# Kernel tuning notes

Hardware: AMD Instinct MI355X
Metric: run time of the kernel (lower is better)

Reference implementation:

```python
import jax, jax.numpy as jnp
import numpy as np

U, D, B, E, H = 128, 256, 1024, 64, 8
EPS_LN = 1e-5
FS0 = 1.0 / 137.036


def _ln(h, g, b):
    m = h.mean(-1, keepdims=True)
    v = jnp.var(h, axis=-1, keepdims=True)
    return (h - m) * jax.lax.rsqrt(v + EPS_LN) * g + b


def setup_inputs() -> dict:
    key = jax.random.key(0)
    ks = iter(jax.random.split(key, 40))

    def n(shape, s=0.05):
        return jax.random.normal(next(ks), shape, jnp.float32) * s

    return dict(
        x=jax.random.normal(next(ks), (B, D), jnp.float32),
        fs=FS0 + n((U,), 0.001),                                   # fine_structure per universe
        dm=-0.1 * jnp.log(jax.random.uniform(next(ks), (U,), jnp.float32, 1e-6, 1.0)),  # Exp(0.1)
        W1=n((U, D, 256)), b1=n((U, 256)), g1=jnp.ones((U, 256), jnp.float32), be1=jnp.zeros((U, 256), jnp.float32),
        W2=n((U, 256, 128)), b2=n((U, 128)), g2=jnp.ones((U, 128), jnp.float32), be2=jnp.zeros((U, 128), jnp.float32),
        W3=n((U, 128, E)), b3=n((U, E)),
        Wr=n((U, E, E)), br=n((U, E)),
        Wa1=n((U, E, 32)), ba1=n((U, 32)),
        Wa2=n((U, 32, 16)), ba2=n((U, 16)),
        Wa3=n((U, 16, 1)), ba3=n((U, 1)),
        Wqkv=n((3 * E, E)), bqkv=n((3 * E,)), Wo=n((E, E)), bo=n((E,)),
        Wc1=n((U, U // 2)), bc1=n((U // 2,)),
        Wc2=n((U // 2, U // 4)), bc2=n((U // 4,)),
        Wc3=n((U // 4, 1)), bc3=n((1,)),
    )


def reference(x, fs, dm, W1, b1, g1, be1, W2, b2, g2, be2, W3, b3, Wr, br,
              Wa1, ba1, Wa2, ba2, Wa3, ba3, Wqkv, bqkv, Wo, bo,
              Wc1, bc1, Wc2, bc2, Wc3, bc3):
    # --- 128 universes batched as one axis (replaces Python loop over UniverseHypothesis) ---
    corr = fs / FS0  # fine-structure correction; x_scaled = x*corr folded into linear output
    h = jnp.einsum('bd,udh->buh', x, W1) * corr[None, :, None] + b1[None]
    h = jax.nn.relu(_ln(h, g1, be1))                     # Dropout(0.1) identity in eval
    h = jax.nn.relu(_ln(jnp.einsum('buh,uhk->buk', h, W2) + b2[None], g2, be2))
    enc = jnp.einsum('buh,uhk->buk', h, W3) + b3[None]   # [B,U,64]
    re = jnp.einsum('bue,uef->buf', enc, Wr) + br[None]
    dmi = jnp.tanh(dm[None, :, None] * jnp.sum(enc * enc, -1, keepdims=True))
    a = jax.nn.relu(jnp.einsum('bue,uef->buf', re + dmi * enc, Wa1) + ba1[None])
    a = jax.nn.relu(jnp.einsum('bue,uef->buf', a, Wa2) + ba2[None])
    scores = jax.nn.sigmoid(jnp.einsum('bue,uef->buf', a, Wa3) + ba3[None])[..., 0]  # [B,U]
    # --- dimensional coupling: MHA self-attention over universe axis (decoherence dropout = eval identity) ---
    b_, u_, e_ = enc.shape
    hd = e_ // H
    qkv = jnp.einsum('bue,fe->buf', enc, Wqkv) + bqkv
    q, k, v = jnp.split(qkv, 3, axis=-1)
    q = q.reshape(b_, u_, H, hd); k = k.reshape(b_, u_, H, hd); v = v.reshape(b_, u_, H, hd)
    attn = jax.nn.softmax(jnp.einsum('bqhd,bkhd->bhqk', q, k) / jnp.sqrt(jnp.float32(hd)), axis=-1)
    coupled = jnp.einsum('bhqk,bkhd->bqhd', attn, v).reshape(b_, u_, e_)
    coupled = jnp.einsum('bue,fe->buf', coupled, Wo) + bo   # computed as in torch, unused downstream
    attn_w = attn.mean(axis=1)                              # torch MHA averages heads -> [B,U,U]
    # --- consensus fusion ---
    cons = jax.nn.relu(scores @ Wc1 + bc1)
    cons = jax.nn.relu(cons @ Wc2 + bc2)
    cons = jax.nn.sigmoid(cons @ Wc3 + bc3)                 # [B,1]
    weighted = scores * attn_w.mean(axis=1)                 # mean over query dim
    mva = jnp.sum(weighted * cons, axis=-1, keepdims=True)  # [B,1]
    collapse = (cons > 0.95).astype(jnp.float32)
    std = jnp.std(scores, axis=-1, ddof=1, keepdims=True)   # torch.std is unbiased
    mean = jnp.mean(scores, axis=-1, keepdims=True)
    agree = 1.0 - std / (mean + 1e-8)
    n_active = jnp.sum(scores > 0.1, axis=-1).astype(jnp.float32)
    return (mva, collapse, agree, cons, attn_w.mean(), n_active)
```

## Files before the change

### kernel.cpp

```cpp
#include <hip/hip_runtime.h>
#include <math.h>


typedef float f32x4 __attribute__((ext_vector_type(4)));
typedef int   i32x4 __attribute__((ext_vector_type(4)));

__device__ __forceinline__ void mfma_bf16(f32x4& c, i32x4 a, i32x4 b) {
    asm("v_mfma_f32_16x16x32_bf16 %0, %1, %2, %0" : "+v"(c) : "v"(a), "v"(b));
}

__device__ __forceinline__ void gl_lds16(const void* g, void* l) {
    __builtin_amdgcn_global_load_lds(
        (const __attribute__((address_space(1))) unsigned int*)g,
        (__attribute__((address_space(3))) unsigned int*)l, 16, 0, 0);
}

__device__ __forceinline__ unsigned short f2bf(float v) {
    union { __bf16 b; unsigned short u; } cv;
    cv.b = (__bf16)v;
    return cv.u;
}

__global__ __launch_bounds__(256)
void prep_kernel(const float* __restrict__ W1, const float* __restrict__ W2,
                 const float* __restrict__ W3, const float* __restrict__ Wr,
                 const float* __restrict__ x, const float* __restrict__ Wqkv,
                 unsigned short* __restrict__ W1t, unsigned short* __restrict__ W2t,
                 unsigned short* __restrict__ W3t, unsigned short* __restrict__ Wrt,
                 unsigned short* __restrict__ xb, unsigned short* __restrict__ wqkvb)
{
    const int bid = blockIdx.x, t = threadIdx.x;
    if (bid >= 3456) {
        const float* src; unsigned short* dst; int base;
        if (bid >= 3584) { src = Wqkv; dst = wqkvb; base = (bid - 3584) * 2048 + t * 8; }
        else             { src = x;    dst = xb;    base = (bid - 3456) * 2048 + t * 8; }
        const float4 v0 = *(const float4*)(src + base);
        const float4 v1 = *(const float4*)(src + base + 4);
        __align__(16) unsigned short o[8];
        o[0]=f2bf(v0.x); o[1]=f2bf(v0.y); o[2]=f2bf(v0.z); o[3]=f2bf(v0.w);
        o[4]=f2bf(v1.x); o[5]=f2bf(v1.y); o[6]=f2bf(v1.z); o[7]=f2bf(v1.w);
        *(uint4*)(dst + base) = *(const uint4*)o;
        return;
    }
    const float* src; unsigned short* dst; int u, k0, n0, N, ktiles;
    if (bid < 2048)      { u = bid >> 4;        int tl = bid & 15;       k0 = (tl>>2)*64; n0 = (tl&3)*64; N=256; ktiles=8; src = W1 + (size_t)u*65536; dst = W1t + (size_t)u*65536; }
    else if (bid < 3072) { int b2 = bid - 2048; u = b2 >> 3; int tl = b2 & 7; k0 = (tl>>1)*64; n0 = (tl&1)*64; N=128; ktiles=8; src = W2 + (size_t)u*32768; dst = W2t + (size_t)u*32768; }
    else if (bid < 3328) { int b3 = bid - 3072; u = b3 >> 1; int tl = b3 & 1; k0 = tl*64;      n0 = 0;         N=64;  ktiles=4; src = W3 + (size_t)u*8192;  dst = W3t + (size_t)u*8192;  }
    else                 { u = bid - 3328;      k0 = 0; n0 = 0;                                 N=64;  ktiles=2; src = Wr + (size_t)u*4096;  dst = Wrt + (size_t)u*4096;  }

    __shared__ unsigned short tile[64 * 65];
    #pragma unroll
    for (int i = 0; i < 16; ++i) {
        const int e = i * 256 + t;
        const int kk = e >> 6, nn = e & 63;
        tile[kk * 65 + nn] = f2bf(src[(size_t)(k0 + kk) * N + n0 + nn]);
    }
    __syncthreads();
    #pragma unroll
    for (int i = 0; i < 16; ++i) {
        const int e = i * 256 + t;
        const int nn = e >> 6, kk = e & 63;
        const int n = n0 + nn, k = k0 + kk;
        dst[(size_t)(((n >> 4) * ktiles + (k >> 5)) * 512 + (n & 15) * 32 + (k & 31))] = tile[kk * 65 + nn];
    }
}

__global__ __launch_bounds__(256, 4)
void fused_mfma(const unsigned short* __restrict__ xb,
                const unsigned short* __restrict__ W1t, const unsigned short* __restrict__ W2t,
                const unsigned short* __restrict__ W3t, const unsigned short* __restrict__ Wrt,
                const float* __restrict__ fs, const float* __restrict__ dm,
                const float* __restrict__ b1, const float* __restrict__ g1, const float* __restrict__ be1,
                const float* __restrict__ b2, const float* __restrict__ g2, const float* __restrict__ be2,
                const float* __restrict__ b3, const float* __restrict__ br,
                const float* __restrict__ Wa1, const float* __restrict__ ba1,
                const float* __restrict__ Wa2, const float* __restrict__ ba2,
                const float* __restrict__ Wa3, const float* __restrict__ ba3,
                unsigned short* __restrict__ enc_bfg, float* __restrict__ scores_g)
{
    __shared__ __align__(128) char sm[39680];
    char* R0 = sm;
    float* pS = (float*)(sm + 36864);
    float* pQ = (float*)(sm + 37888);
    float2* rst = (float2*)(sm + 38912);
    float* dmis = (float*)(sm + 39424);

    const int t = threadIdx.x;
    const int wid = t >> 6, lane = t & 63, l15 = lane & 15, lk = lane >> 4;
    const int swz = (l15 & 7) << 4;
    const int lo64 = l15 * 64 + lk * 16;
    const int bx = blockIdx.x;
    const int xcd = bx & 7, idx = bx >> 3;
    const int u = ((idx >> 4) << 3) + xcd;
    const int b0 = (idx & 15) * 64;

    const float corru = fs[u] * 137.036f;
    const float dmu = dm[u];

    const char* xbase = (const char*)xb + (size_t)b0 * 512;
    const char* w1u = (const char*)W1t + (size_t)u * 131072;
    const char* w2u = (const char*)W2t + (size_t)u * 65536;
    const char* w3u = (const char*)W3t + (size_t)u * 16384;
    const char* wru = (const char*)Wrt + (size_t)u * 8192;

    #pragma unroll
    for (int it = 0; it < 8; ++it) {
        const int d = it * 4096 + t * 16;
        const int s = d ^ (((d >> 9) & 7) << 4);
        gl_lds16(xbase + s, R0 + it * 4096 + wid * 1024);
    }
    __syncthreads();

    const f32x4 z4 = {0.f, 0.f, 0.f, 0.f};
    f32x4 acc[4][4];
    #pragma unroll
    for (int mi = 0; mi < 4; ++mi)
        #pragma unroll
        for (int ni = 0; ni < 4; ++ni) acc[mi][ni] = z4;

    {
        i32x4 bfP[4], bfQ[4];
        #pragma unroll
        for (int ni = 0; ni < 4; ++ni)
            bfP[ni] = *(const i32x4*)(w1u + ((wid * 4 + ni) * 8 + 0) * 1024 + lo64);
        #pragma unroll
        for (int kt = 0; kt < 8; ++kt) {
            if (kt < 7) {
                #pragma unroll
                for (int ni = 0; ni < 4; ++ni)
                    ((kt & 1) ? bfP : bfQ)[ni] =
                        *(const i32x4*)(w1u + ((wid * 4 + ni) * 8 + kt + 1) * 1024 + lo64);
            }
            i32x4 af[4];
            const int p = kt >> 1, ks = kt & 1;
            #pragma unroll
            for (int mi = 0; mi < 4; ++mi) {
                const int off = ((mi * 16 + l15) << 9) + p * 128 + ks * 64 + lk * 16;
                af[mi] = *(const i32x4*)(R0 + (off ^ swz));
            }
            #pragma unroll
            for (int mi = 0; mi < 4; ++mi)
                #pragma unroll
                for (int ni = 0; ni < 4; ++ni)
                    mfma_bf16(acc[mi][ni], af[mi], ((kt & 1) ? bfQ : bfP)[ni]);
        }
    }

    float bb[4], gg[4], ee[4];
    #pragma unroll
    for (int ni = 0; ni < 4; ++ni) {
        const int c = wid * 64 + ni * 16 + l15;
        bb[ni] = b1[u * 256 + c]; gg[ni] = g1[u * 256 + c]; ee[ni] = be1[u * 256 + c];
    }
    #pragma unroll
    for (int mi = 0; mi < 4; ++mi) {
        #pragma unroll
        for (int j = 0; j < 4; ++j) {
            float s = 0.f, q = 0.f;
            #pragma unroll
            for (int ni = 0; ni < 4; ++ni) {
                const float h = acc[mi][ni][j] * corru + bb[ni];
                acc[mi][ni][j] = h;
                s += h; q += h * h;
            }
            #pragma unroll
            for (int m = 1; m < 16; m <<= 1) { s += __shfl_xor(s, m); q += __shfl_xor(q, m); }
            if (l15 == 0) {
                const int r = mi * 16 + lk * 4 + j;
                pS[wid * 64 + r] = s; pQ[wid * 64 + r] = q;
            }
        }
    }
    __syncthreads();
    if (t < 64) {
        const float s = pS[t] + pS[64 + t] + pS[128 + t] + pS[192 + t];
        const float q = pQ[t] + pQ[64 + t] + pQ[128 + t] + pQ[192 + t];
        const float mean = s * (1.f / 256.f);
        const float var = fmaxf(q * (1.f / 256.f) - mean * mean, 0.f);
        rst[t] = make_float2(mean, rsqrtf(var + 1e-5f));
    }
    __syncthreads();
    #pragma unroll
    for (int mi = 0; mi < 4; ++mi) {
        #pragma unroll
        for (int j = 0; j < 4; ++j) {
            const int r = mi * 16 + lk * 4 + j;
            const float2 st = rst[r];
            #pragma unroll
            for (int ni = 0; ni < 4; ++ni) {
                const float h = fmaxf((acc[mi][ni][j] - st.x) * st.y * gg[ni] + ee[ni], 0.f);
                const int c = wid * 64 + ni * 16 + l15;
                const int off = (r << 9) + c * 2;
                *(__bf16*)(R0 + (off ^ ((r & 7) << 4))) = (__bf16)h;
            }
        }
    }
    __syncthreads();

    f32x4 acc2[4][2];
    #pragma unroll
    for (int mi = 0; mi < 4; ++mi) { acc2[mi][0] = z4; acc2[mi][1] = z4; }
    {
        i32x4 bfP[2], bfQ[2];
        #pragma unroll
        for (int ni = 0; ni < 2; ++ni)
            bfP[ni] = *(const i32x4*)(w2u + ((wid * 2 + ni) * 8 + 0) * 1024 + lo64);
        #pragma unroll
        for (int kt = 0; kt < 8; ++kt) {
            if (kt < 7) {
                #pragma unroll
                for (int ni = 0; ni < 2; ++ni)
                    ((kt & 1) ? bfP : bfQ)[ni] =
                        *(const i32x4*)(w2u + ((wid * 2 + ni) * 8 + kt + 1) * 1024 + lo64);
            }
            i32x4 af[4];
            const int p = kt >> 1, ks = kt & 1;
            #pragma unroll
            for (int mi = 0; mi < 4; ++mi) {
                const int off = ((mi * 16 + l15) << 9) + p * 128 + ks * 64 + lk * 16;
                af[mi] = *(const i32x4*)(R0 + (off ^ swz));
            }
            #pragma unroll
            for (int mi = 0; mi < 4; ++mi)
                #pragma unroll
                for (int ni = 0; ni < 2; ++ni)
                    mfma_bf16(acc2[mi][ni], af[mi], ((kt & 1) ? bfQ : bfP)[ni]);
        }
    }

    float bb2[2], gg2[2], ee2[2];
    #pragma unroll
    for (int ni = 0; ni < 2; ++ni) {
        const int c = wid * 32 + ni * 16 + l15;
        bb2[ni] = b2[u * 128 + c]; gg2[ni] = g2[u * 128 + c]; ee2[ni] = be2[u * 128 + c];
    }
    #pragma unroll
    for (int mi = 0; mi < 4; ++mi) {
        #pragma unroll
        for (int j = 0; j < 4; ++j) {
            float s = 0.f, q = 0.f;
            #pragma unroll
            for (int ni = 0; ni < 2; ++ni) {
                const float h = acc2[mi][ni][j] + bb2[ni];
                acc2[mi][ni][j] = h;
                s += h; q += h * h;
            }
            #pragma unroll
            for (int m = 1; m < 16; m <<= 1) { s += __shfl_xor(s, m); q += __shfl_xor(q, m); }
            if (l15 == 0) {
                const int r = mi * 16 + lk * 4 + j;
                pS[wid * 64 + r] = s; pQ[wid * 64 + r] = q;
            }
        }
    }
    __syncthreads();
    if (t < 64) {
        const float s = pS[t] + pS[64 + t] + pS[128 + t] + pS[192 + t];
        const float q = pQ[t] + pQ[64 + t] + pQ[128 + t] + pQ[192 + t];
        const float mean = s * (1.f / 128.f);
        const float var = fmaxf(q * (1.f / 128.f) - mean * mean, 0.f);
        rst[t] = make_float2(mean, rsqrtf(var + 1e-5f));
    }
    __syncthreads();
    #pragma unroll
    for (int mi = 0; mi < 4; ++mi) {
        #pragma unroll
        for (int j = 0; j < 4; ++j) {
            const int r = mi * 16 + lk * 4 + j;
            const float2 st = rst[r];
            #pragma unroll
            for (int ni = 0; ni < 2; ++ni) {
                const float h = fmaxf((acc2[mi][ni][j] - st.x) * st.y * gg2[ni] + ee2[ni], 0.f);
                const int c = wid * 32 + ni * 16 + l15;
                const int off = (r << 8) + c * 2;
                *(__bf16*)(R0 + (off ^ ((r & 7) << 4))) = (__bf16)h;
            }
        }
    }
    __syncthreads();

    f32x4 acc3[4];
    #pragma unroll
    for (int mi = 0; mi < 4; ++mi) acc3[mi] = z4;
    #pragma unroll
    for (int ks = 0; ks < 4; ++ks) {
        const i32x4 bfr = *(const i32x4*)(w3u + (wid * 4 + ks) * 1024 + lo64);
        #pragma unroll
        for (int mi = 0; mi < 4; ++mi) {
            const int off = ((mi * 16 + l15) << 8) + ks * 64 + lk * 16;
            const i32x4 afm = *(const i32x4*)(R0 + (off ^ swz));
            mfma_bf16(acc3[mi], afm, bfr);
        }
    }
    const int c16 = wid * 16 + l15;
    const float b3v = b3[u * 64 + c16];
    float encr[4][4];
    #pragma unroll
    for (int mi = 0; mi < 4; ++mi) {
        #pragma unroll
        for (int j = 0; j < 4; ++j) {
            const float e = acc3[mi][j] + b3v;
            encr[mi][j] = e;
            float q = e * e;
            #pragma unroll
            for (int m = 1; m < 16; m <<= 1) q += __shfl_xor(q, m);
            if (l15 == 0) {
                const int r = mi * 16 + lk * 4 + j;
                pQ[wid * 64 + r] = q;
            }
        }
    }
    __syncthreads();
    if (t < 64) {
        const float q = pQ[t] + pQ[64 + t] + pQ[128 + t] + pQ[192 + t];
        dmis[t] = tanhf(dmu * q);
    }
    #pragma unroll
    for (int mi = 0; mi < 4; ++mi) {
        #pragma unroll
        for (int j = 0; j < 4; ++j) {
            const int r = mi * 16 + lk * 4 + j;
            const int off = (r << 7) + c16 * 2;
            *(__bf16*)(R0 + (off ^ ((r & 7) << 4))) = (__bf16)encr[mi][j];
        }
    }
    __syncthreads();

    {
        const int c8 = t & 7;
        #pragma unroll
        for (int pass = 0; pass < 2; ++pass) {
            const int row = pass * 32 + (t >> 3);
            const int off = (row << 7) + c8 * 16;
            const uint4 v = *(const uint4*)(R0 + (off ^ ((row & 7) << 4)));
            *(uint4*)((char*)enc_bfg + (((size_t)(b0 + row) * 128 + u) << 7) + c8 * 16) = v;
        }
    }

    f32x4 accR[4];
    #pragma unroll
    for (int mi = 0; mi < 4; ++mi) accR[mi] = z4;
    #pragma unroll
    for (int ks = 0; ks < 2; ++ks) {
        const i32x4 bfr = *(const i32x4*)(wru + (wid * 2 + ks) * 1024 + lo64);
        #pragma unroll
        for (int mi = 0; mi < 4; ++mi) {
            const int off = ((mi * 16 + l15) << 7) + ks * 64 + lk * 16;
            const i32x4 afm = *(const i32x4*)(R0 + (off ^ swz));
            mfma_bf16(accR[mi], afm, bfr);
        }
    }
    const float brv = br[u * 64 + c16];
    #pragma unroll
    for (int mi = 0; mi < 4; ++mi) {
        #pragma unroll
        for (int j = 0; j < 4; ++j) {
            const int r = mi * 16 + lk * 4 + j;
            const float zv = accR[mi][j] + brv + dmis[r] * encr[mi][j];
            *(float*)(R0 + 8192 + r * 272 + c16 * 4) = zv;
        }
    }
    __syncthreads();

    #pragma unroll
    for (int it = 0; it < 2; ++it)
        gl_lds16((const char*)Wa1 + (size_t)u * 8192 + it * 4096 + t * 16,
                 R0 + it * 4096 + wid * 1024);
    if (t < 128)
        gl_lds16((const char*)Wa2 + (size_t)u * 2048 + t * 16, R0 + 25600 + wid * 1024);
    if (t < 16) ((float*)(R0 + 27648))[t] = Wa3[u * 16 + t];
    if (t == 16) ((float*)(R0 + 27648))[16] = ba3[u];
    __syncthreads();

    {
        const int row = t >> 2, g4 = t & 3;
        float accA[8] = {0.f,0.f,0.f,0.f,0.f,0.f,0.f,0.f};
        const float* zrow = (const float*)(R0 + 8192 + row * 272);
        const float* wa1s = (const float*)R0;
        for (int k = 0; k < 64; ++k) {
            const float zv = zrow[k];
            const float4 wA = *(const float4*)(wa1s + k * 32 + g4 * 8);
            const float4 wB = *(const float4*)(wa1s + k * 32 + g4 * 8 + 4);
            accA[0] += zv * wA.x; accA[1] += zv * wA.y; accA[2] += zv * wA.z; accA[3] += zv * wA.w;
            accA[4] += zv * wB.x; accA[5] += zv * wB.y; accA[6] += zv * wB.z; accA[7] += zv * wB.w;
        }
        const float4 bA = *(const float4*)(ba1 + u * 32 + g4 * 8);
        const float4 bB = *(const float4*)(ba1 + u * 32 + g4 * 8 + 4);
        float* a1s = (float*)(R0 + 28160);
        a1s[row * 34 + g4 * 8 + 0] = fmaxf(accA[0] + bA.x, 0.f);
        a1s[row * 34 + g4 * 8 + 1] = fmaxf(accA[1] + bA.y, 0.f);
        a1s[row * 34 + g4 * 8 + 2] = fmaxf(accA[2] + bA.z, 0.f);
        a1s[row * 34 + g4 * 8 + 3] = fmaxf(accA[3] + bA.w, 0.f);
        a1s[row * 34 + g4 * 8 + 4] = fmaxf(accA[4] + bB.x, 0.f);
        a1s[row * 34 + g4 * 8 + 5] = fmaxf(accA[5] + bB.y, 0.f);
        a1s[row * 34 + g4 * 8 + 6] = fmaxf(accA[6] + bB.z, 0.f);
        a1s[row * 34 + g4 * 8 + 7] = fmaxf(accA[7] + bB.w, 0.f);
    }
    __syncthreads();

    {
        const int row = t >> 2, g4 = t & 3;
        const float* a1s = (const float*)(R0 + 28160);
        const float* wa2s = (const float*)(R0 + 25600);
        float accB[4] = {0.f,0.f,0.f,0.f};
        for (int k = 0; k < 32; ++k) {
            const float av = a1s[row * 34 + k];
            const float4 w = *(const float4*)(wa2s + k * 16 + g4 * 4);
            accB[0] += av * w.x; accB[1] += av * w.y; accB[2] += av * w.z; accB[3] += av * w.w;
        }
        const float4 bB = *(const float4*)(ba2 + u * 16 + g4 * 4);
        float* a2s = (float*)R0;
        a2s[row * 18 + g4 * 4 + 0] = fmaxf(accB[0] + bB.x, 0.f);
        a2s[row * 18 + g4 * 4 + 1] = fmaxf(accB[1] + bB.y, 0.f);
        a2s[row * 18 + g4 * 4 + 2] = fmaxf(accB[2] + bB.z, 0.f);
        a2s[row * 18 + g4 * 4 + 3] = fmaxf(accB[3] + bB.w, 0.f);
    }
    __syncthreads();

    if (t < 64) {
        const float* a2s = (const float*)R0;
        const float* w3s = (const float*)(R0 + 27648);
        float a = w3s[16];
        #pragma unroll
        for (int k = 0; k < 16; ++k) a += a2s[t * 18 + k] * w3s[k];
        scores_g[(size_t)u * 1024 + b0 + t] = 1.f / (1.f + __expf(-a));
    }
}

__global__ __launch_bounds__(256, 3)
void attn_kernel(const unsigned short* __restrict__ enc_bf,
                 const unsigned short* __restrict__ wqkv_bf,
                 const float* __restrict__ bqkv, float* __restrict__ smean,
                 float* __restrict__ bpart)
{
    __shared__ __align__(128) char sm[34944];
    char* Qp = sm;
    char* Ks = sm + 16384;
    float* colp = (float*)(sm + 32832);
    char* ENCs = sm;
    char* WQs  = sm + 16384;

    const int t = threadIdx.x;
    const int wid = t >> 6, lane = t & 63, l15 = lane & 15, lk = lane >> 4;
    const int swz = (l15 & 7) << 4;
    const int b = blockIdx.x;

    const char* eb = (const char*)(enc_bf + (size_t)b * 8192);
    #pragma unroll
    for (int it = 0; it < 4; ++it) {
        const int d = it * 4096 + t * 16;
        const int s = d ^ (((d >> 7) & 7) << 4);
        gl_lds16(eb + s, ENCs + it * 4096 + wid * 1024);
    }
    const char* wb = (const char*)wqkv_bf;
    #pragma unroll
    for (int it = 0; it < 4; ++it) {
        const int d = it * 4096 + t * 16;
        const int s = d ^ (((d >> 7) & 7) << 4);
        gl_lds16(wb + s, WQs + it * 4096 + wid * 1024);
    }
    __syncthreads();

    const f32x4 z4 = {0.f,0.f,0.f,0.f};
    f32x4 aq[2][4], ak[2][4];
    #pragma unroll
    for (int mi = 0; mi < 2; ++mi)
        #pragma unroll
        for (int ni = 0; ni < 4; ++ni) { aq[mi][ni] = z4; ak[mi][ni] = z4; }

    i32x4 af[2][2];
    #pragma unroll
    for (int mi = 0; mi < 2; ++mi)
        #pragma unroll
        for (int ks = 0; ks < 2; ++ks) {
            const int off = ((wid * 32 + mi * 16 + l15) << 7) + ks * 64 + lk * 16;
            af[mi][ks] = *(const i32x4*)(ENCs + (off ^ swz));
        }
    #pragma unroll
    for (int ni = 0; ni < 4; ++ni)
        #pragma unroll
        for (int ks = 0; ks < 2; ++ks) {
            const int offq = ((ni * 16 + l15) << 7) + ks * 64 + lk * 16;
            const i32x4 bq = *(const i32x4*)(WQs + (offq ^ swz));
            mfma_bf16(aq[0][ni], af[0][ks], bq);
            mfma_bf16(aq[1][ni], af[1][ks], bq);
            const i32x4 bk = *(const i32x4*)(WQs + ((offq + 8192) ^ swz));
            mfma_bf16(ak[0][ni], af[0][ks], bk);
            mfma_bf16(ak[1][ni], af[1][ks], bk);
        }

    float bqv[4], bkv[4];
    #pragma unroll
    for (int ni = 0; ni < 4; ++ni) {
        bqv[ni] = bqkv[ni * 16 + l15];
        bkv[ni] = bqkv[64 + ni * 16 + l15];
    }
    __syncthreads();

    {
        const int par = t >> 7, row = t & 127;
        char* base = Qp + par * 8192 + row * 64;
        *(f32x4*)(base + 16) = z4;
        *(f32x4*)(base + 32) = z4;
        *(f32x4*)(base + 48) = z4;
    }
    #pragma unroll
    for (int mi = 0; mi < 2; ++mi)
        #pragma unroll
        for (int ni = 0; ni < 4; ++ni)
            #pragma unroll
            for (int j = 0; j < 4; ++j) {
                const int row = wid * 32 + mi * 16 + lk * 4 + j;
                const int f = ni * 16 + l15;
                const int off = row * 128 + f * 2;
                *(__bf16*)(Ks + (off ^ ((row & 7) << 4))) = (__bf16)(ak[mi][ni][j] + bkv[ni]);
            }
    __syncthreads();

    const float qscale = 0.35355339059327373f;
    float cp[8] = {0.f,0.f,0.f,0.f,0.f,0.f,0.f,0.f};

    #pragma unroll
    for (int p = 0; p < 4; ++p) {
        #pragma unroll
        for (int mi = 0; mi < 2; ++mi)
            #pragma unroll
            for (int j = 0; j < 4; ++j) {
                const int row = wid * 32 + mi * 16 + lk * 4 + j;
                *(__bf16*)(Qp + (l15 >> 3) * 8192 + row * 64 + (l15 & 7) * 2) =
                    (__bf16)((aq[mi][p][j] + bqv[p]) * qscale);
            }
        __syncthreads();

        #pragma unroll 1
        for (int par = 0; par < 2; ++par) {
            const int h = p * 2 + par;
            const i32x4 aQ0 = *(const i32x4*)(Qp + par * 8192 + (wid * 32 + l15) * 64 + lk * 16);
            const i32x4 aQ1 = *(const i32x4*)(Qp + par * 8192 + (wid * 32 + 16 + l15) * 64 + lk * 16);
            f32x4 accS[2][8];
            #pragma unroll
            for (int ci = 0; ci < 8; ++ci) { accS[0][ci] = z4; accS[1][ci] = z4; }
            #pragma unroll
            for (int ci = 0; ci < 8; ++ci) {
                const int col = ci * 16 + l15;
                const i32x4 bK = *(const i32x4*)(Ks + ((col * 128 + ((h + lk) & 7) * 16) ^ ((col & 7) << 4)));
                mfma_bf16(accS[0][ci], aQ0, bK);
                mfma_bf16(accS[1][ci], aQ1, bK);
            }
            #pragma unroll
            for (int mi = 0; mi < 2; ++mi)
                #pragma unroll
                for (int j = 0; j < 4; ++j) {
                    float e[8];
                    float z = 0.f;
                    #pragma unroll
                    for (int ci = 0; ci < 8; ++ci) { e[ci] = __expf(accS[mi][ci][j]); z += e[ci]; }
                    z += __shfl_xor(z, 1); z += __shfl_xor(z, 2);
                    z += __shfl_xor(z, 4); z += __shfl_xor(z, 8);
                    const float zi = 1.f / z;
                    #pragma unroll
                    for (int ci = 0; ci < 8; ++ci) cp[ci] += e[ci] * zi;
                }
        }
        __syncthreads();
    }

    #pragma unroll
    for (int ci = 0; ci < 8; ++ci) {
        cp[ci] += __shfl_xor(cp[ci], 16);
        cp[ci] += __shfl_xor(cp[ci], 32);
    }
    if (lk == 0) {
        #pragma unroll
        for (int ci = 0; ci < 8; ++ci)
            colp[wid * 128 + ci * 16 + l15] = cp[ci];
    }
    __syncthreads();
    float v = 0.f;
    if (t < 128) {
        v = colp[t] + colp[128 + t] + colp[256 + t] + colp[384 + t];
        smean[(size_t)b * 128 + t] = v * (1.f / 1024.f);
    }
    #pragma unroll
    for (int m = 1; m < 64; m <<= 1) v += __shfl_xor(v, m);
    if (lane == 0) colp[512 + wid] = v;
    __syncthreads();
    if (t == 0)
        bpart[b] = (colp[512] + colp[513] + colp[514] + colp[515]) * (1.f / 1024.f);
}

__global__ __launch_bounds__(64)
void final_kernel(const float* __restrict__ scores_g, const float* __restrict__ smean,
                  const float* __restrict__ Wc1, const float* __restrict__ bc1,
                  const float* __restrict__ Wc2, const float* __restrict__ bc2,
                  const float* __restrict__ Wc3, const float* __restrict__ bc3,
                  float* __restrict__ out)
{
    __shared__ float sc[128];
    __shared__ float c1[64];
    __shared__ float c2[32];
    const int b = blockIdx.x, t = threadIdx.x;
    const float s0 = scores_g[(size_t)t * 1024 + b];
    const float s1 = scores_g[(size_t)(t + 64) * 1024 + b];
    sc[t] = s0; sc[64 + t] = s1;
    const float v0 = smean[(size_t)b * 128 + t];
    const float v1 = smean[(size_t)b * 128 + 64 + t];
    __syncthreads();
    float a = bc1[t];
    #pragma unroll 8
    for (int i = 0; i < 128; ++i) a += sc[i] * Wc1[i * 64 + t];
    c1[t] = fmaxf(a, 0.f);
    __syncthreads();
    if (t < 32) {
        float a2 = bc2[t];
        #pragma unroll 8
        for (int i = 0; i < 64; ++i) a2 += c1[i] * Wc2[i * 32 + t];
        c2[t] = fmaxf(a2, 0.f);
    }
    __syncthreads();
    float p = (t < 32) ? c2[t] * Wc3[t] : 0.f;
    #pragma unroll
    for (int m = 1; m < 64; m <<= 1) p += __shfl_xor(p, m);
    const float cons = 1.f / (1.f + __expf(-(p + bc3[0])));

    float sum = s0 + s1;
    float sq  = s0 * s0 + s1 * s1;
    float wsm = s0 * v0 + s1 * v1;
    float na  = (s0 > 0.1f ? 1.f : 0.f) + (s1 > 0.1f ? 1.f : 0.f);
    #pragma unroll
    for (int m = 1; m < 64; m <<= 1) {
        sum += __shfl_xor(sum, m); sq += __shfl_xor(sq, m);
        wsm += __shfl_xor(wsm, m); na += __shfl_xor(na, m);
    }
    if (t == 0) {
        const float mean = sum * (1.f / 128.f);
        float var = (sq - 128.f * mean * mean) * (1.f / 127.f);
        var = fmaxf(var, 0.f);
        const float agree = 1.f - sqrtf(var) / (mean + 1e-8f);
        out[b]        = cons * wsm;
        out[1024 + b] = (cons > 0.95f) ? 1.f : 0.f;
        out[2048 + b] = agree;
        out[3072 + b] = cons;
        out[4097 + b] = na;
    }
}

__global__ __launch_bounds__(256)
void attnmean_kernel(const float* __restrict__ bpart, float* __restrict__ out)
{
    __shared__ float red[4];
    const int t = threadIdx.x;
    const int lane = t & 63, wid = t >> 6;
    float s = bpart[t] + bpart[256 + t] + bpart[512 + t] + bpart[768 + t];
    #pragma unroll
    for (int m = 1; m < 64; m <<= 1) s += __shfl_xor(s, m);
    if (lane == 0) red[wid] = s;
    __syncthreads();
    if (t == 0) out[4096] = (red[0] + red[1] + red[2] + red[3]) * (1.f / 131072.f);
}

extern "C" void kernel_launch(void* const* d_in, const int* in_sizes, int n_in,
                              void* d_out, int out_size, void* d_ws, size_t ws_size,
                              hipStream_t stream)
{
    const float* x    = (const float*)d_in[0];
    const float* fs   = (const float*)d_in[1];
    const float* dm   = (const float*)d_in[2];
    const float* W1   = (const float*)d_in[3];
    const float* b1   = (const float*)d_in[4];
    const float* g1   = (const float*)d_in[5];
    const float* be1  = (const float*)d_in[6];
    const float* W2   = (const float*)d_in[7];
    const float* b2   = (const float*)d_in[8];
    const float* g2   = (const float*)d_in[9];
    const float* be2  = (const float*)d_in[10];
    const float* W3   = (const float*)d_in[11];
    const float* b3   = (const float*)d_in[12];
    const float* Wr   = (const float*)d_in[13];
    const float* br   = (const float*)d_in[14];
    const float* Wa1  = (const float*)d_in[15];
    const float* ba1  = (const float*)d_in[16];
    const float* Wa2  = (const float*)d_in[17];
    const float* ba2  = (const float*)d_in[18];
    const float* Wa3  = (const float*)d_in[19];
    const float* ba3  = (const float*)d_in[20];
    const float* Wqkv = (const float*)d_in[21];
    const float* bqkv = (const float*)d_in[22];
    const float* Wc1  = (const float*)d_in[25];
    const float* bc1  = (const float*)d_in[26];
    const float* Wc2  = (const float*)d_in[27];
    const float* bc2  = (const float*)d_in[28];
    const float* Wc3  = (const float*)d_in[29];
    const float* bc3  = (const float*)d_in[30];

    float* out = (float*)d_out;
    char*  ws8 = (char*)d_ws;
    unsigned short* enc_bf = (unsigned short*)ws8;
    float* scores = (float*)(ws8 + 16777216);
    float* smean  = (float*)(ws8 + 17301504);
    float* bpart  = (float*)(ws8 + 17825792);
    unsigned short* xb    = (unsigned short*)(ws8 + 17829888);
    unsigned short* W1t   = (unsigned short*)(ws8 + 18354176);
    unsigned short* W2t   = (unsigned short*)(ws8 + 35131392);
    unsigned short* W3t   = (unsigned short*)(ws8 + 43520000);
    unsigned short* Wrt   = (unsigned short*)(ws8 + 45617152);
    unsigned short* wqkvb = (unsigned short*)(ws8 + 46665728);

    prep_kernel<<<3588, 256, 0, stream>>>(W1, W2, W3, Wr, x, Wqkv,
                                          W1t, W2t, W3t, Wrt, xb, wqkvb);
    fused_mfma<<<2048, 256, 0, stream>>>(xb, W1t, W2t, W3t, Wrt, fs, dm,
                                         b1, g1, be1, b2, g2, be2, b3, br,
                                         Wa1, ba1, Wa2, ba2, Wa3, ba3,
                                         enc_bf, scores);
    attn_kernel<<<1024, 256, 0, stream>>>(enc_bf, wqkvb, bqkv, smean, bpart);
    final_kernel<<<1024, 64, 0, stream>>>(scores, smean, Wc1, bc1, Wc2, bc2, Wc3, bc3, out);
    attnmean_kernel<<<1, 256, 0, stream>>>(bpart, out);
}
```

Before: 149.0 us.

## Move anomaly MLP head to split-bf16 MFMA and use DPP row reductions

The two small anomaly-detector layers (Wa1, Wa2) in the fused kernel move from scalar FP32 loops over LDS to MFMA instructions. Activations and weights are split into high and low bf16 parts, and three MFMAs per product keep near-FP32 accuracy. The weights are pre-split and re-laid out in the prep kernel. The final 16-wide dot and the sigmoid become a register reduction, which removes several LDS staging passes and barriers. Shuffle-based 16-lane reductions are replaced with DPP row operations in the layernorm, encoder-norm and softmax paths. The cost is extra prep work and extra MFMA issue for the precision split.

```diff
diff --git a/kernel.cpp b/kernel.cpp
--- a/kernel.cpp
+++ b/kernel.cpp
@@ -20,16 +20,59 @@
     cv.b = (__bf16)v;
     return cv.u;
 }
+__device__ __forceinline__ float bf2f(unsigned short u) {
+    union { unsigned int i; float f; } c; c.i = (unsigned int)u << 16; return c.f;
+}
+
+__device__ __forceinline__ float red16(float v) {
+    int x;
+    x = __builtin_amdgcn_update_dpp(0, __float_as_int(v), 0xB1, 0xF, 0xF, true);
+    v += __int_as_float(x);
+    x = __builtin_amdgcn_update_dpp(0, __float_as_int(v), 0x4E, 0xF, 0xF, true);
+    v += __int_as_float(x);
+    x = __builtin_amdgcn_update_dpp(0, __float_as_int(v), 0x124, 0xF, 0xF, true);
+    v += __int_as_float(x);
+    x = __builtin_amdgcn_update_dpp(0, __float_as_int(v), 0x128, 0xF, 0xF, true);
+    v += __int_as_float(x);
+    return v;
+}
 
 __global__ __launch_bounds__(256)
 void prep_kernel(const float* __restrict__ W1, const float* __restrict__ W2,
                  const float* __restrict__ W3, const float* __restrict__ Wr,
+                 const float* __restrict__ Wa1, const float* __restrict__ Wa2,
                  const float* __restrict__ x, const float* __restrict__ Wqkv,
                  unsigned short* __restrict__ W1t, unsigned short* __restrict__ W2t,
                  unsigned short* __restrict__ W3t, unsigned short* __restrict__ Wrt,
+                 unsigned short* __restrict__ Wa1t, unsigned short* __restrict__ Wa2t,
                  unsigned short* __restrict__ xb, unsigned short* __restrict__ wqkvb)
 {
     const int bid = blockIdx.x, t = threadIdx.x;
+    if (bid >= 3588) {
+        const int uu = bid - 3588;
+        #pragma unroll
+        for (int i = 0; i < 8; ++i) {
+            const int e = t * 8 + i;
+            const int k = e >> 5, n = e & 31;
+            const float v = Wa1[(size_t)uu * 2048 + k * 32 + n];
+            const unsigned short h = f2bf(v);
+            const unsigned short l = f2bf(v - bf2f(h));
+            const size_t d = (size_t)uu * 4096 +
+                (((n >> 4) * 2 + (k >> 5)) * 512 + (n & 15) * 32 + (k & 31));
+            Wa1t[d] = h; Wa1t[d + 2048] = l;
+        }
+        #pragma unroll
+        for (int i = 0; i < 2; ++i) {
+            const int e = t * 2 + i;
+            const int k = e >> 4, n = e & 15;
+            const float v = Wa2[(size_t)uu * 512 + k * 16 + n];
+            const unsigned short h = f2bf(v);
+            const unsigned short l = f2bf(v - bf2f(h));
+            const size_t d = (size_t)uu * 1024 + n * 32 + k;
+            Wa2t[d] = h; Wa2t[d + 512] = l;
+        }
+        return;
+    }
     if (bid >= 3456) {
         const float* src; unsigned short* dst; int base;
         if (bid >= 3584) { src = Wqkv; dst = wqkvb; base = (bid - 3584) * 2048 + t * 8; }
@@ -69,12 +112,12 @@
 void fused_mfma(const unsigned short* __restrict__ xb,
                 const unsigned short* __restrict__ W1t, const unsigned short* __restrict__ W2t,
                 const unsigned short* __restrict__ W3t, const unsigned short* __restrict__ Wrt,
+                const unsigned short* __restrict__ Wa1t, const unsigned short* __restrict__ Wa2t,
                 const float* __restrict__ fs, const float* __restrict__ dm,
                 const float* __restrict__ b1, const float* __restrict__ g1, const float* __restrict__ be1,
                 const float* __restrict__ b2, const float* __restrict__ g2, const float* __restrict__ be2,
                 const float* __restrict__ b3, const float* __restrict__ br,
-                const float* __restrict__ Wa1, const float* __restrict__ ba1,
-                const float* __restrict__ Wa2, const float* __restrict__ ba2,
+                const float* __restrict__ ba1, const float* __restrict__ ba2,
                 const float* __restrict__ Wa3, const float* __restrict__ ba3,
                 unsigned short* __restrict__ enc_bfg, float* __restrict__ scores_g)
 {
@@ -102,6 +145,8 @@
     const char* w2u = (const char*)W2t + (size_t)u * 65536;
     const char* w3u = (const char*)W3t + (size_t)u * 16384;
     const char* wru = (const char*)Wrt + (size_t)u * 8192;
+    const char* wa1u = (const char*)Wa1t + (size_t)u * 8192;
+    const char* wa2u = (const char*)Wa2t + (size_t)u * 2048;
 
     #pragma unroll
     for (int it = 0; it < 8; ++it) {
@@ -163,8 +208,7 @@
                 acc[mi][ni][j] = h;
                 s += h; q += h * h;
             }
-            #pragma unroll
-            for (int m = 1; m < 16; m <<= 1) { s += __shfl_xor(s, m); q += __shfl_xor(q, m); }
+            s = red16(s); q = red16(q);
             if (l15 == 0) {
                 const int r = mi * 16 + lk * 4 + j;
                 pS[wid * 64 + r] = s; pQ[wid * 64 + r] = q;
@@ -245,8 +289,7 @@
                 acc2[mi][ni][j] = h;
                 s += h; q += h * h;
             }
-            #pragma unroll
-            for (int m = 1; m < 16; m <<= 1) { s += __shfl_xor(s, m); q += __shfl_xor(q, m); }
+            s = red16(s); q = red16(q);
             if (l15 == 0) {
                 const int r = mi * 16 + lk * 4 + j;
                 pS[wid * 64 + r] = s; pQ[wid * 64 + r] = q;
@@ -301,9 +344,7 @@
         for (int j = 0; j < 4; ++j) {
             const float e = acc3[mi][j] + b3v;
             encr[mi][j] = e;
-            float q = e * e;
-            #pragma unroll
-            for (int m = 1; m < 16; m <<= 1) q += __shfl_xor(q, m);
+            const float q = red16(e * e);
             if (l15 == 0) {
                 const int r = mi * 16 + lk * 4 + j;
                 pQ[wid * 64 + r] = q;
@@ -357,73 +398,71 @@
         for (int j = 0; j < 4; ++j) {
             const int r = mi * 16 + lk * 4 + j;
             const float zv = accR[mi][j] + brv + dmis[r] * encr[mi][j];
-            *(float*)(R0 + 8192 + r * 272 + c16 * 4) = zv;
-        }
-    }
-    __syncthreads();
-
-    #pragma unroll
-    for (int it = 0; it < 2; ++it)
-        gl_lds16((const char*)Wa1 + (size_t)u * 8192 + it * 4096 + t * 16,
-                 R0 + it * 4096 + wid * 1024);
-    if (t < 128)
-        gl_lds16((const char*)Wa2 + (size_t)u * 2048 + t * 16, R0 + 25600 + wid * 1024);
-    if (t < 16) ((float*)(R0 + 27648))[t] = Wa3[u * 16 + t];
-    if (t == 16) ((float*)(R0 + 27648))[16] = ba3[u];
-    __syncthreads();
-
+            const __bf16 zh = (__bf16)zv;
+            const __bf16 zl = (__bf16)(zv - (float)zh);
+            const int off = (r << 7) + c16 * 2;
+            const int sw = (r & 7) << 4;
+            *(__bf16*)(R0 + 8192 + (off ^ sw)) = zh;
+            *(__bf16*)(R0 + 16384 + (off ^ sw)) = zl;
+        }
+    }
+    __syncthreads();
+
+    f32x4 accA[2] = {z4, z4};
+    #pragma unroll
+    for (int ks = 0; ks < 2; ++ks) {
+        const int zoff = ((wid * 16 + l15) << 7) + ks * 64 + lk * 16;
+        const int zsw = (l15 & 7) << 4;
+        const i32x4 zh = *(const i32x4*)(R0 + 8192 + (zoff ^ zsw));
+        const i32x4 zl = *(const i32x4*)(R0 + 16384 + (zoff ^ zsw));
+        #pragma unroll
+        for (int ni = 0; ni < 2; ++ni) {
+            const i32x4 bh = *(const i32x4*)(wa1u + (ni * 2 + ks) * 1024 + lo64);
+            const i32x4 bl = *(const i32x4*)(wa1u + 4096 + (ni * 2 + ks) * 1024 + lo64);
+            mfma_bf16(accA[ni], zh, bh);
+            mfma_bf16(accA[ni], zl, bh);
+            mfma_bf16(accA[ni], zh, bl);
+        }
+    }
+    #pragma unroll
+    for (int ni = 0; ni < 2; ++ni) {
+        const float bav = ba1[u * 32 + ni * 16 + l15];
+        #pragma unroll
+        for (int j = 0; j < 4; ++j) {
+            const int row = wid * 16 + lk * 4 + j;
+            const float av = fmaxf(accA[ni][j] + bav, 0.f);
+            const __bf16 ah = (__bf16)av;
+            const __bf16 al = (__bf16)(av - (float)ah);
+            const int off = (row << 6) + (ni * 16 + l15) * 2;
+            const int sw = (row & 3) << 4;
+            *(__bf16*)(R0 + 24576 + (off ^ sw)) = ah;
+            *(__bf16*)(R0 + 28672 + (off ^ sw)) = al;
+        }
+    }
+
+    f32x4 accB = z4;
     {
-        const int row = t >> 2, g4 = t & 3;
-        float accA[8] = {0.f,0.f,0.f,0.f,0.f,0.f,0.f,0.f};
-        const float* zrow = (const float*)(R0 + 8192 + row * 272);
-        const float* wa1s = (const float*)R0;
-        for (int k = 0; k < 64; ++k) {
-            const float zv = zrow[k];
-            const float4 wA = *(const float4*)(wa1s + k * 32 + g4 * 8);
-            const float4 wB = *(const float4*)(wa1s + k * 32 + g4 * 8 + 4);
-            accA[0] += zv * wA.x; accA[1] += zv * wA.y; accA[2] += zv * wA.z; accA[3] += zv * wA.w;
-            accA[4] += zv * wB.x; accA[5] += zv * wB.y; accA[6] += zv * wB.z; accA[7] += zv * wB.w;
-        }
-        const float4 bA = *(const float4*)(ba1 + u * 32 + g4 * 8);
-        const float4 bB = *(const float4*)(ba1 + u * 32 + g4 * 8 + 4);
-        float* a1s = (float*)(R0 + 28160);
-        a1s[row * 34 + g4 * 8 + 0] = fmaxf(accA[0] + bA.x, 0.f);
-        a1s[row * 34 + g4 * 8 + 1] = fmaxf(accA[1] + bA.y, 0.f);
-        a1s[row * 34 + g4 * 8 + 2] = fmaxf(accA[2] + bA.z, 0.f);
-        a1s[row * 34 + g4 * 8 + 3] = fmaxf(accA[3] + bA.w, 0.f);
-        a1s[row * 34 + g4 * 8 + 4] = fmaxf(accA[4] + bB.x, 0.f);
-        a1s[row * 34 + g4 * 8 + 5] = fmaxf(accA[5] + bB.y, 0.f);
-        a1s[row * 34 + g4 * 8 + 6] = fmaxf(accA[6] + bB.z, 0.f);
-        a1s[row * 34 + g4 * 8 + 7] = fmaxf(accA[7] + bB.w, 0.f);
-    }
-    __syncthreads();
-
-    {
-        const int row = t >> 2, g4 = t & 3;
-        const float* a1s = (const float*)(R0 + 28160);
-        const float* wa2s = (const float*)(R0 + 25600);
-        float accB[4] = {0.f,0.f,0.f,0.f};
-        for (int k = 0; k < 32; ++k) {
-            const float av = a1s[row * 34 + k];
-            const float4 w = *(const float4*)(wa2s + k * 16 + g4 * 4);
-            accB[0] += av * w.x; accB[1] += av * w.y; accB[2] += av * w.z; accB[3] += av * w.w;
-        }
-        const float4 bB = *(const float4*)(ba2 + u * 16 + g4 * 4);
-        float* a2s = (float*)R0;
-        a2s[row * 18 + g4 * 4 + 0] = fmaxf(accB[0] + bB.x, 0.f);
-        a2s[row * 18 + g4 * 4 + 1] = fmaxf(accB[1] + bB.y, 0.f);
-        a2s[row * 18 + g4 * 4 + 2] = fmaxf(accB[2] + bB.z, 0.f);
-        a2s[row * 18 + g4 * 4 + 3] = fmaxf(accB[3] + bB.w, 0.f);
-    }
-    __syncthreads();
-
-    if (t < 64) {
-        const float* a2s = (const float*)R0;
-        const float* w3s = (const float*)(R0 + 27648);
-        float a = w3s[16];
-        #pragma unroll
-        for (int k = 0; k < 16; ++k) a += a2s[t * 18 + k] * w3s[k];
-        scores_g[(size_t)u * 1024 + b0 + t] = 1.f / (1.f + __expf(-a));
+        const int row = wid * 16 + l15;
+        const int aoff = (row << 6) + lk * 16;
+        const int asw = (l15 & 3) << 4;
+        const i32x4 ah = *(const i32x4*)(R0 + 24576 + (aoff ^ asw));
+        const i32x4 al = *(const i32x4*)(R0 + 28672 + (aoff ^ asw));
+        const i32x4 bh = *(const i32x4*)(wa2u + lo64);
+        const i32x4 bl = *(const i32x4*)(wa2u + 1024 + lo64);
+        mfma_bf16(accB, ah, bh);
+        mfma_bf16(accB, al, bh);
+        mfma_bf16(accB, ah, bl);
+    }
+    const float ba2v = ba2[u * 16 + l15];
+    const float wa3v = Wa3[u * 16 + l15];
+    const float ba3u = ba3[u];
+    #pragma unroll
+    for (int j = 0; j < 4; ++j) {
+        const float vsum = red16(fmaxf(accB[j] + ba2v, 0.f) * wa3v);
+        if (l15 == 0) {
+            const int r = wid * 16 + lk * 4 + j;
+            scores_g[(size_t)u * 1024 + b0 + r] = 1.f / (1.f + __expf(-(vsum + ba3u)));
+        }
     }
 }
 
@@ -555,8 +594,7 @@
                     float z = 0.f;
                     #pragma unroll
                     for (int ci = 0; ci < 8; ++ci) { e[ci] = __expf(accS[mi][ci][j]); z += e[ci]; }
-                    z += __shfl_xor(z, 1); z += __shfl_xor(z, 2);
-                    z += __shfl_xor(z, 4); z += __shfl_xor(z, 8);
+                    z = red16(z);
                     const float zi = 1.f / z;
                     #pragma unroll
                     for (int ci = 0; ci < 8; ++ci) cp[ci] += e[ci] * zi;
@@ -705,12 +743,14 @@
     unsigned short* W3t   = (unsigned short*)(ws8 + 43520000);
     unsigned short* Wrt   = (unsigned short*)(ws8 + 45617152);
     unsigned short* wqkvb = (unsigned short*)(ws8 + 46665728);
-
-    prep_kernel<<<3588, 256, 0, stream>>>(W1, W2, W3, Wr, x, Wqkv,
-                                          W1t, W2t, W3t, Wrt, xb, wqkvb);
-    fused_mfma<<<2048, 256, 0, stream>>>(xb, W1t, W2t, W3t, Wrt, fs, dm,
+    unsigned short* Wa1t  = (unsigned short*)(ws8 + 46682112);
+    unsigned short* Wa2t  = (unsigned short*)(ws8 + 47730688);
+
+    prep_kernel<<<3716, 256, 0, stream>>>(W1, W2, W3, Wr, Wa1, Wa2, x, Wqkv,
+                                          W1t, W2t, W3t, Wrt, Wa1t, Wa2t, xb, wqkvb);
+    fused_mfma<<<2048, 256, 0, stream>>>(xb, W1t, W2t, W3t, Wrt, Wa1t, Wa2t, fs, dm,
                                          b1, g1, be1, b2, g2, be2, b3, br,
-                                         Wa1, ba1, Wa2, ba2, Wa3, ba3,
+                                         ba1, ba2, Wa3, ba3,
                                          enc_bf, scores);
     attn_kernel<<<1024, 256, 0, stream>>>(enc_bf, wqkvb, bqkv, smean, bpart);
     final_kernel<<<1024, 64, 0, stream>>>(scores, smean, Wc1, bc1, Wc2, bc2, Wc3, bc3, out);
```

After: 121.5 us, median of 4. 18.5% less time.
